# Optimization experiments

Hardware: AMD Instinct MI355X
Metric: run time of the kernel (lower is better)

The kernel has to match this reference:

```python
import jax, jax.numpy as jnp
import numpy as np

N, E, R = 30000, 480000, 8192
N_IN, E_IN = 128, 64
N_HID, E_HID = 256, 128
N_OUT, E_OUT = 256, 64
N_CLASS, N_COL = 10, 128
NEG = 0.01  # LeakyReLU slope


def leaky(x):
    return jnp.where(x > 0, x, NEG * x)


def pe_init(n_pos, d):
    # sinusoid position encoding table (position_encoding_init)
    pe = np.array([[p / np.power(10000, 2 * (j // 2) / d) for j in range(d)]
                   if p != 0 else np.zeros(d) for p in range(n_pos)])
    pe[1:, 0::2] = np.sin(pe[1:, 0::2])
    pe[1:, 1::2] = np.cos(pe[1:, 1::2])
    return jnp.asarray(pe, jnp.float32)


def segment_mean(vals, idx, n):
    s = jax.ops.segment_sum(vals, idx, num_segments=n)
    c = jax.ops.segment_sum(jnp.ones((vals.shape[0], 1), vals.dtype), idx, num_segments=n)
    return s / jnp.maximum(c, 1.0)


def esage(x, e, src, dst, We, be, Wn, bn):
    # edge update from [x_src ; e], mean-aggregate messages to dst nodes, node update
    e2 = leaky(jnp.concatenate([x[src], e], axis=-1) @ We + be)      # [E, e_out]
    h = segment_mean(e2, dst, x.shape[0])                             # [N, e_out]
    x2 = leaky(jnp.concatenate([x, h], axis=-1) @ Wn + bn)            # [N, n_out]
    return x2, e2


def setup_inputs():
    key = jax.random.key(0)
    ks = jax.random.split(key, 24)

    def xav(k, shp):
        std = float(np.sqrt(2.0 / (shp[0] + shp[1])))
        return jax.random.normal(k, shp, jnp.float32) * std

    return {
        'x': jax.random.normal(ks[0], (N, N_IN), jnp.float32),
        'e': jax.random.normal(ks[1], (E, E_IN), jnp.float32),
        'src': jax.random.randint(ks[2], (E,), 0, N),
        'dst': jax.random.randint(ks[3], (E,), 0, N),
        'row_idx': jax.random.randint(ks[4], (R,), 0, N),
        'col_idx': jax.random.randint(ks[5], (N_COL,), 0, N),
        'real': jax.random.normal(ks[6], (R * N_COL, E_OUT), jnp.float32),
        'mask': jax.random.randint(ks[7], (R, N_COL), 0, 2) == 1,
        'W1e': xav(ks[8], (N_IN + E_IN, E_HID)), 'b1e': jnp.zeros((E_HID,), jnp.float32),
        'W1n': xav(ks[9], (N_IN + E_HID, N_HID)), 'b1n': jnp.zeros((N_HID,), jnp.float32),
        'W2e': xav(ks[10], (N_HID + E_HID, E_OUT)), 'b2e': jnp.zeros((E_OUT,), jnp.float32),
        'W2n': xav(ks[11], (N_HID + E_OUT, N_OUT)), 'b2n': jnp.zeros((N_OUT,), jnp.float32),
        'node_pe': pe_init(N_COL, N_HID),
        'Wq': xav(ks[12], (N_HID, N_HID)),
        'Wk': xav(ks[13], (N_HID, N_HID)),
        'Wv': xav(ks[14], (N_HID, N_HID)),
        'Wref': xav(ks[15], (N_HID, N_HID)), 'bref': jnp.zeros((N_HID,), jnp.float32),
        'Wr': xav(ks[16], (N_OUT, E_OUT)),
        'Wc': xav(ks[17], (N_HID, E_OUT)), 'bep': jnp.zeros((E_OUT,), jnp.float32),
        'Wcls': xav(ks[18], (N_COL * E_OUT, N_CLASS)), 'bcls': jnp.zeros((N_CLASS,), jnp.float32),
    }


def reference(x, e, src, dst, row_idx, col_idx, real, mask,
              W1e, b1e, W1n, b1n, W2e, b2e, W2n, b2n,
              node_pe, Wq, Wk, Wv, Wref, bref, Wr, Wc, bep, Wcls, bcls):
    # two ESAGE message-passing layers
    x1, e1 = esage(x, e, src, dst, W1e, b1e, W1n, b1n)
    new_col = x1[col_idx]                                  # [C, n_hidden]
    x2, e2 = esage(x1, e1, src, dst, W2e, b2e, W2n, b2n)
    new_row = x2[row_idx]                                  # [R, n_out]

    # node self-attention (hand-rolled, incl. the duplicated dist@v from the source)
    c = new_col + node_pe
    q, k, v = c @ Wq, c @ Wk, c @ Wv
    dist = jax.nn.softmax((q @ k.T) * (1.0 / np.sqrt(N_HID)), axis=-1)
    c = 2.0 * (dist @ v)                                    # mm(dist,v) + mm(dist,v)
    new_col = jax.nn.sigmoid(c @ Wref + bref)

    # edge predictor over all (row, col) pairs: [R, C, e_out]
    pred = leaky((new_row @ Wr)[:, None, :] + (new_col @ Wc)[None, :, :] + bep)
    pred_flat = pred.reshape(R * N_COL, E_OUT)

    # masked imputation: real where mask True, predicted elsewhere
    imput_e = jnp.where(mask.reshape(-1)[:, None], real, pred_flat)
    imput_e = imput_e.reshape(R, N_COL, E_OUT)

    # mlp classifier: Flatten -> Linear -> LogSoftmax
    res = jax.nn.log_softmax(imput_e.reshape(R, -1) @ Wcls + bcls, axis=-1)
    return (res, pred_flat)
```

## Files before the change

kernel.cpp:

```cpp
#include <hip/hip_runtime.h>
#include <hip/hip_bf16.h>
#include <math.h>

#define NNODES 30000
#define NEDGES 480000
#define RROWS  8192
#define NCOLS  128
#define NIN    128
#define EIN    64
#define NHID   256
#define EHID   128
#define NOUTD  256
#define EOUTD  64
#define NCLS   10
#define NB_PFX 118

typedef __attribute__((ext_vector_type(8))) unsigned short ushort8;
typedef __attribute__((ext_vector_type(8))) short bhalf8;
typedef __attribute__((ext_vector_type(4))) float floatx4;

__device__ __forceinline__ float lrelu(float v){ return v > 0.f ? v : 0.01f * v; }
__device__ __forceinline__ float4 ld4(const float* p){ return *(const float4*)p; }
__device__ __forceinline__ float4 ntld4(const float* p){
    floatx4 v = __builtin_nontemporal_load((const floatx4*)p);
    return make_float4(v.x, v.y, v.z, v.w);
}
__device__ __forceinline__ void ntst4(float* p, float4 v){
    floatx4 n = {v.x, v.y, v.z, v.w};
    __builtin_nontemporal_store(n, (floatx4*)p);
}
__device__ __forceinline__ void ntst8u(unsigned short* p, ushort8 v){
    __builtin_nontemporal_store(v, (ushort8*)p);
}
__device__ __forceinline__ unsigned short f2b(float f){
    unsigned int u = __builtin_bit_cast(unsigned int, f);
    u += 0x7fffu + ((u >> 16) & 1u);
    return (unsigned short)(u >> 16);
}
__device__ __forceinline__ float b2f(unsigned short b){
    unsigned int u = ((unsigned int)b) << 16;
    return __builtin_bit_cast(float, u);
}

#define PREP_CVT_N   1875
#define PREP_W1T_B   (PREP_CVT_N)
#define PREP_W1B_B   (PREP_W1T_B + 64)
#define PREP_W2T_B   (PREP_W1B_B + 32)
#define PREP_W2B_B   (PREP_W2T_B + 64)
#define PREP_W1N_B   (PREP_W2B_B + 32)
#define PREP_W2N_B   (PREP_W1N_B + 256)
#define PREP_HIST_B  (PREP_W2N_B + 320)
#define PREP_DET_B   (PREP_HIST_B + 1875)
#define PREP_TOTAL   (PREP_DET_B + 1)

__device__ __forceinline__ void wT_region(const float* __restrict__ W, unsigned short* __restrict__ Wt,
                                          int KOFF, int KSUB, int N, int idx){
    if (idx >= N * KSUB) return;
    int n = idx / KSUB, k = idx % KSUB;
    Wt[idx] = f2b(W[(size_t)(KOFF + k) * N + n]);
}

__global__ __launch_bounds__(256) void k_prep(
    const float* __restrict__ x, unsigned short* __restrict__ xb,
    const float* __restrict__ W1e, unsigned short* __restrict__ W1tT, unsigned short* __restrict__ W1bT,
    const float* __restrict__ W2e, unsigned short* __restrict__ W2tT, unsigned short* __restrict__ W2bT,
    const float* __restrict__ W1n, unsigned short* __restrict__ W1nTb,
    const float* __restrict__ W2n, unsigned short* __restrict__ W2nTb,
    const int* __restrict__ dst, int* __restrict__ cnt_i,
    const unsigned int* __restrict__ mask, int* __restrict__ mode)
{
    const int bid = blockIdx.x, t = threadIdx.x;
    if (bid < PREP_CVT_N){
        int i = bid * 256 + t;
        float4 a = ntld4(x + (size_t)i * 8), b = ntld4(x + (size_t)i * 8 + 4);
        ushort8 o = {f2b(a.x), f2b(a.y), f2b(a.z), f2b(a.w), f2b(b.x), f2b(b.y), f2b(b.z), f2b(b.w)};
        *(ushort8*)(xb + (size_t)i * 8) = o;
    } else if (bid < PREP_W1B_B){
        wT_region(W1e, W1tT, 0, 128, 128, (bid - PREP_W1T_B) * 256 + t);
    } else if (bid < PREP_W2T_B){
        wT_region(W1e, W1bT, 128, 64, 128, (bid - PREP_W1B_B) * 256 + t);
    } else if (bid < PREP_W2B_B){
        wT_region(W2e, W2tT, 0, 256, 64, (bid - PREP_W2T_B) * 256 + t);
    } else if (bid < PREP_W1N_B){
        wT_region(W2e, W2bT, 256, 128, 64, (bid - PREP_W2B_B) * 256 + t);
    } else if (bid < PREP_W2N_B){
        wT_region(W1n, W1nTb, 0, 256, 256, (bid - PREP_W1N_B) * 256 + t);
    } else if (bid < PREP_HIST_B){
        wT_region(W2n, W2nTb, 0, 320, 256, (bid - PREP_W2N_B) * 256 + t);
    } else if (bid < PREP_DET_B){
        int i = (bid - PREP_HIST_B) * 256 + t;
        if (i < NEDGES) atomicAdd(&cnt_i[dst[i]], 1);
    } else if (t == 0){
        bool allI32 = true, allF32 = true;
        for (int i = 0; i < 64; i++){
            unsigned int v = mask[i];
            if (!(v == 0u || v == 1u)) allI32 = false;
            if (!(v == 0u || v == 0x3F800000u)) allF32 = false;
        }
        *mode = allI32 ? 0 : (allF32 ? 1 : 2);
    }
}

__global__ __launch_bounds__(256) void k_pfx1(const int* __restrict__ cnt_i, int* __restrict__ blocksum){
    __shared__ int red[256];
    const int t = threadIdx.x;
    const int i = blockIdx.x * 256 + t;
    red[t] = (i < NNODES) ? cnt_i[i] : 0;
    __syncthreads();
    for (int o = 128; o; o >>= 1){ if (t < o) red[t] += red[t + o]; __syncthreads(); }
    if (t == 0) blocksum[blockIdx.x] = red[0];
}
__global__ __launch_bounds__(128) void k_pfx2(const int* __restrict__ blocksum, int* __restrict__ blockoff){
    __shared__ int s[128];
    const int t = threadIdx.x;
    int v = (t < NB_PFX) ? blocksum[t] : 0;
    s[t] = v;
    __syncthreads();
    for (int o = 1; o < 128; o <<= 1){
        int add = (t >= o) ? s[t - o] : 0;
        __syncthreads();
        s[t] += add;
        __syncthreads();
    }
    if (t < NB_PFX) blockoff[t] = s[t] - v;
}
__global__ __launch_bounds__(256) void k_pfx3(const int* __restrict__ cnt_i, const int* __restrict__ blockoff,
                                              int* __restrict__ cursor, float* __restrict__ cntf){
    __shared__ int s[256];
    const int t = threadIdx.x;
    const int i = blockIdx.x * 256 + t;
    int v = (i < NNODES) ? cnt_i[i] : 0;
    s[t] = v;
    __syncthreads();
    for (int o = 1; o < 256; o <<= 1){
        int add = (t >= o) ? s[t - o] : 0;
        __syncthreads();
        s[t] += add;
        __syncthreads();
    }
    if (i < NNODES){
        cursor[i] = s[t] - v + blockoff[blockIdx.x];
        cntf[i] = (float)v;
    }
}

__global__ void k_scatter(const int* __restrict__ dst, int* __restrict__ cursor, int* __restrict__ eidx){
    int i = blockIdx.x * 256 + threadIdx.x;
    if (i >= NEDGES) return;
    int pos = atomicAdd(&cursor[dst[i]], 1);
    eidx[pos] = i;
}
__global__ void k_sgather(const int* __restrict__ src, const int* __restrict__ dst,
                          const int* __restrict__ eidx,
                          int* __restrict__ srcs, int* __restrict__ dsts){
    int p = blockIdx.x * 256 + threadIdx.x;
    if (p >= NEDGES) return;
    int i = eidx[p];
    srcs[p] = src[i];
    dsts[p] = dst[i];
}

template<int K, int N>
__global__ __launch_bounds__(256) void k_gemm_b16(
    const unsigned short* __restrict__ Ab, const unsigned short* __restrict__ Wt,
    unsigned short* __restrict__ outb, int M)
{
    __shared__ unsigned short At[64][K + 8];
    const int t = threadIdx.x;
    const int r0 = blockIdx.x * 64;
    {
        const int r = t >> 2, q = t & 3;
        const int row = r0 + r;
        const bool valid = row < M;
        const unsigned short* a = Ab + (size_t)(valid ? row : 0) * K;
        for (int kk = q * (K / 4); kk < (q + 1) * (K / 4); kk += 8){
            ushort8 u;
            if (valid) u = *(const ushort8*)(a + kk);
            else       u = (ushort8){0,0,0,0,0,0,0,0};
            *(ushort8*)&At[r][kk] = u;
        }
    }
    __syncthreads();
    const int lane = t & 63, w = t >> 6;
    const int fr = lane & 15, fq = lane >> 4;
    constexpr int NF = N / 16;
    floatx4 acc[NF] = {};
    #pragma unroll
    for (int ks = 0; ks < K / 32; ks++){
        const int k = ks * 32 + fq * 8;
        bhalf8 a = *(bhalf8*)&At[w * 16 + fr][k];
        #pragma unroll
        for (int n = 0; n < NF; n++){
            bhalf8 b = *(const bhalf8*)(Wt + (size_t)(n * 16 + fr) * K + k);
            acc[n] = __builtin_amdgcn_mfma_f32_16x16x32_bf16(a, b, acc[n], 0, 0, 0);
        }
    }
    #pragma unroll
    for (int n = 0; n < NF; n++){
        const int col = n * 16 + fr;
        #pragma unroll
        for (int rr = 0; rr < 4; rr++){
            const int row = r0 + w * 16 + fq * 4 + rr;
            if (row < M) outb[(size_t)row * N + col] = f2b(acc[n][rr]);
        }
    }
}

__global__ __launch_bounds__(256) void k_edge1_fused(
    const float* __restrict__ e,
    const int* __restrict__ srcs, const int* __restrict__ dsts, const int* __restrict__ eidx,
    const unsigned short* __restrict__ W1bT, const float* __restrict__ b1e,
    const unsigned short* __restrict__ P1b, const unsigned short* __restrict__ W2bT,
    unsigned short* __restrict__ Qb, float* __restrict__ hsum)
{
    __shared__ unsigned short Cb[64][136];
    __shared__ unsigned short P1s[64][136];
    __shared__ int dstS[64];
    const int t = threadIdx.x;
    const int p0 = blockIdx.x * 64;
    const int r = t >> 2, q = t & 3;
    {
        const int p = p0 + r;
        if (q == 0) dstS[r] = dsts[p];
        const int srow = srcs[p];
        const unsigned short* pp = P1b + (size_t)srow * 128 + q * 32;
        *(ushort8*)&P1s[r][q * 32]      = *(const ushort8*)pp;
        *(ushort8*)&P1s[r][q * 32 + 8]  = *(const ushort8*)(pp + 8);
        *(ushort8*)&P1s[r][q * 32 + 16] = *(const ushort8*)(pp + 16);
        *(ushort8*)&P1s[r][q * 32 + 24] = *(const ushort8*)(pp + 24);
        const int ei = eidx[p];
        const float* ep = e + (size_t)ei * 64 + q * 16;
        float4 f0 = ntld4(ep), f1 = ntld4(ep + 4), f2 = ntld4(ep + 8), f3 = ntld4(ep + 12);
        ushort8 u0 = {f2b(f0.x), f2b(f0.y), f2b(f0.z), f2b(f0.w), f2b(f1.x), f2b(f1.y), f2b(f1.z), f2b(f1.w)};
        ushort8 u1 = {f2b(f2.x), f2b(f2.y), f2b(f2.z), f2b(f2.w), f2b(f3.x), f2b(f3.y), f2b(f3.z), f2b(f3.w)};
        *(ushort8*)&Cb[r][q * 16]     = u0;
        *(ushort8*)&Cb[r][q * 16 + 8] = u1;
    }
    __syncthreads();
    const int lane = t & 63, w = t >> 6;
    const int wm = w >> 1, wn = w & 1;
    const int fr = lane & 15, fq = lane >> 4;
    floatx4 acc1[2][4] = {};
    #pragma unroll
    for (int ks = 0; ks < 2; ks++){
        const int k = ks * 32 + fq * 8;
        bhalf8 a0 = *(bhalf8*)&Cb[wm * 32 + fr][k];
        bhalf8 a1 = *(bhalf8*)&Cb[wm * 32 + 16 + fr][k];
        #pragma unroll
        for (int n = 0; n < 4; n++){
            const int col = wn * 64 + n * 16 + fr;
            bhalf8 b = *(const bhalf8*)(W1bT + (size_t)col * 64 + k);
            acc1[0][n] = __builtin_amdgcn_mfma_f32_16x16x32_bf16(a0, b, acc1[0][n], 0, 0, 0);
            acc1[1][n] = __builtin_amdgcn_mfma_f32_16x16x32_bf16(a1, b, acc1[1][n], 0, 0, 0);
        }
    }
    __syncthreads();
    #pragma unroll
    for (int m = 0; m < 2; m++){
        #pragma unroll
        for (int n = 0; n < 4; n++){
            const int col = wn * 64 + n * 16 + fr;
            const float bv = b1e[col];
            #pragma unroll
            for (int rr = 0; rr < 4; rr++){
                const int row = wm * 32 + m * 16 + fq * 4 + rr;
                const float pv = b2f(P1s[row][col]);
                Cb[row][col] = f2b(lrelu(acc1[m][n][rr] + pv + bv));
            }
        }
    }
    __syncthreads();
    {
        floatx4 acc2[4] = {};
        #pragma unroll
        for (int ks = 0; ks < 4; ks++){
            const int k = ks * 32 + fq * 8;
            bhalf8 a = *(bhalf8*)&Cb[w * 16 + fr][k];
            #pragma unroll
            for (int n = 0; n < 4; n++){
                bhalf8 b = *(const bhalf8*)(W2bT + (size_t)(n * 16 + fr) * 128 + k);
                acc2[n] = __builtin_amdgcn_mfma_f32_16x16x32_bf16(a, b, acc2[n], 0, 0, 0);
            }
        }
        #pragma unroll
        for (int n = 0; n < 4; n++){
            const int col = n * 16 + fr;
            #pragma unroll
            for (int rr = 0; rr < 4; rr++){
                const int row = w * 16 + fq * 4 + rr;
                P1s[row][col] = f2b(acc2[n][rr]);
            }
        }
    }
    __syncthreads();
    {
        unsigned short* op = Qb + (size_t)(p0 + r) * 64 + q * 16;
        ntst8u(op,     *(ushort8*)&P1s[r][q * 16]);
        ntst8u(op + 8, *(ushort8*)&P1s[r][q * 16 + 8]);
    }
    {
        const int col = t & 127, half = t >> 7;
        const int rbase = half * 32;
        float s = 0.f;
        int prev = dstS[rbase];
        #pragma unroll 4
        for (int rr = 0; rr < 32; rr++){
            const int rw2 = rbase + rr;
            const int d = dstS[rw2];
            if (d != prev){
                atomicAdd(&hsum[(size_t)prev * EHID + col], s);
                s = 0.f; prev = d;
            }
            s += b2f(Cb[rw2][col]);
        }
        atomicAdd(&hsum[(size_t)prev * EHID + col], s);
    }
}

__global__ __launch_bounds__(256) void k_edge2_lite(
    const unsigned short* __restrict__ P2b, const unsigned short* __restrict__ Qb,
    const int* __restrict__ srcs, const int* __restrict__ dsts,
    const float* __restrict__ b2e, float* __restrict__ hsum)
{
    const int t = threadIdx.x;
    const int lane = t & 63, w = t >> 6;
    const int p0 = blockIdx.x * 256 + w * 64;
    const float bias = b2e[lane];
    float s = 0.f;
    int prev = dsts[p0];
    #pragma unroll 4
    for (int i = 0; i < 64; i++){
        const int p = p0 + i;
        const int d = dsts[p];
        if (d != prev){
            atomicAdd(&hsum[(size_t)prev * EOUTD + lane], s);
            s = 0.f; prev = d;
        }
        const float q  = b2f(__builtin_nontemporal_load(&Qb[(size_t)p * 64 + lane]));
        const float pv = b2f(P2b[(size_t)srcs[p] * 64 + lane]);
        s += lrelu(pv + q + bias);
    }
    atomicAdd(&hsum[(size_t)prev * EOUTD + lane], s);
}

template<int K1, int K2, bool WRITE_BF16>
__global__ __launch_bounds__(256) void k_node_mfma(
    const unsigned short* __restrict__ A1b, const float* __restrict__ hsum,
    const float* __restrict__ cntf,
    const unsigned short* __restrict__ Wt, const float* __restrict__ bias,
    float* __restrict__ outf, unsigned short* __restrict__ outb, int M)
{
    constexpr int K = K1 + K2;
    __shared__ unsigned short At[32][K + 8];
    const int t = threadIdx.x;
    const int r0 = blockIdx.x * 32;
    {
        const int r = t >> 3, q = t & 7;
        const int row = r0 + r;
        const bool valid = row < M;
        float rinv = 0.f;
        const unsigned short* a1 = A1b;
        const float* a2 = hsum;
        if (valid){
            rinv = 1.f / fmaxf(cntf[row], 1.f);
            a1 = A1b  + (size_t)row * K1;
            a2 = hsum + (size_t)row * K2;
        }
        for (int kk = q * (K / 8); kk < (q + 1) * (K / 8); kk += 8){
            ushort8 u;
            if (!valid){
                u = (ushort8){0,0,0,0,0,0,0,0};
            } else if (kk < K1){
                u = *(const ushort8*)(a1 + kk);
            } else {
                float4 f0 = ld4(a2 + (kk - K1)), f1 = ld4(a2 + (kk - K1) + 4);
                u = (ushort8){f2b(f0.x*rinv), f2b(f0.y*rinv), f2b(f0.z*rinv), f2b(f0.w*rinv),
                              f2b(f1.x*rinv), f2b(f1.y*rinv), f2b(f1.z*rinv), f2b(f1.w*rinv)};
            }
            *(ushort8*)&At[r][kk] = u;
        }
    }
    __syncthreads();
    const int lane = t & 63, w = t >> 6;
    const int wm = w >> 1, wn = w & 1;
    const int fr = lane & 15, fq = lane >> 4;
    floatx4 acc[8] = {};
    #pragma unroll
    for (int ks = 0; ks < K / 32; ks++){
        const int k = ks * 32 + fq * 8;
        bhalf8 a = *(bhalf8*)&At[wm * 16 + fr][k];
        #pragma unroll
        for (int n = 0; n < 8; n++){
            const int col = wn * 128 + n * 16 + fr;
            bhalf8 b = *(const bhalf8*)(Wt + (size_t)col * K + k);
            acc[n] = __builtin_amdgcn_mfma_f32_16x16x32_bf16(a, b, acc[n], 0, 0, 0);
        }
    }
    #pragma unroll
    for (int n = 0; n < 8; n++){
        const int col = wn * 128 + n * 16 + fr;
        const float bv = bias[col];
        #pragma unroll
        for (int rr = 0; rr < 4; rr++){
            const int row = r0 + wm * 16 + fq * 4 + rr;
            if (row < M){
                float o = lrelu(acc[n][rr] + bv);
                outf[(size_t)row * 256 + col] = o;
                if (WRITE_BF16) outb[(size_t)row * 256 + col] = f2b(o);
            }
        }
    }
}

__global__ __launch_bounds__(256) void k_attn_qkv(
    const float* __restrict__ x1, const int* __restrict__ col_idx,
    const float* __restrict__ pe,
    const float* __restrict__ Wq, const float* __restrict__ Wk, const float* __restrict__ Wv,
    float* __restrict__ qo, float* __restrict__ ko, float* __restrict__ vo)
{
    __shared__ float c[256];
    const int i = blockIdx.x, t = threadIdx.x;
    const int col = col_idx[i];
    c[t] = x1[(size_t)col * 256 + t] + pe[i * 256 + t];
    __syncthreads();
    float aq = 0.f, ak = 0.f, av = 0.f;
    #pragma unroll 4
    for (int kk = 0; kk < 256; kk++){
        float cv = c[kk];
        aq += cv * Wq[kk * 256 + t];
        ak += cv * Wk[kk * 256 + t];
        av += cv * Wv[kk * 256 + t];
    }
    qo[i * 256 + t] = aq; ko[i * 256 + t] = ak; vo[i * 256 + t] = av;
}

__global__ __launch_bounds__(128) void k_attn_dist(
    const float* __restrict__ q, const float* __restrict__ k, float* __restrict__ dist)
{
    __shared__ float qr[256];
    __shared__ float red[128];
    const int i = blockIdx.x, t = threadIdx.x;
    qr[t] = q[i * 256 + t]; qr[t + 128] = q[i * 256 + t + 128];
    __syncthreads();
    float s = 0.f;
    #pragma unroll 4
    for (int kk = 0; kk < 256; kk++) s += qr[kk] * k[t * 256 + kk];
    s *= 0.0625f;
    red[t] = s; __syncthreads();
    for (int off = 64; off; off >>= 1){ if (t < off) red[t] = fmaxf(red[t], red[t + off]); __syncthreads(); }
    float m = red[0]; __syncthreads();
    float ex = expf(s - m);
    red[t] = ex; __syncthreads();
    for (int off = 64; off; off >>= 1){ if (t < off) red[t] += red[t + off]; __syncthreads(); }
    dist[i * 128 + t] = ex / red[0];
}

__global__ __launch_bounds__(256) void k_attn_out(
    const float* __restrict__ dist, const float* __restrict__ v,
    const float* __restrict__ Wref, const float* __restrict__ bref,
    const float* __restrict__ Wc, const float* __restrict__ bep,
    float* __restrict__ colWc)
{
    __shared__ float dr[128];
    __shared__ float c2[256];
    __shared__ float nc[256];
    const int i = blockIdx.x, t = threadIdx.x;
    if (t < 128) dr[t] = dist[i * 128 + t];
    __syncthreads();
    float s = 0.f;
    #pragma unroll 4
    for (int j = 0; j < 128; j++) s += dr[j] * v[j * 256 + t];
    c2[t] = 2.f * s;
    __syncthreads();
    float a = 0.f;
    #pragma unroll 4
    for (int kk = 0; kk < 256; kk++) a += c2[kk] * Wref[kk * 256 + t];
    a += bref[t];
    nc[t] = 1.f / (1.f + expf(-a));
    __syncthreads();
    if (t < 64){
        float o = 0.f;
        #pragma unroll 4
        for (int kk = 0; kk < 256; kk++) o += nc[kk] * Wc[kk * 64 + t];
        colWc[i * 64 + t] = o + bep[t];
    }
}

__global__ __launch_bounds__(256) void k_rowwr(
    const float* __restrict__ x2, const int* __restrict__ row_idx,
    const float* __restrict__ Wr, float* __restrict__ rw)
{
    __shared__ float A[16][260];
    const int t = threadIdx.x;
    const int r0 = blockIdx.x * 16;
    const int rl = t >> 4, cg = t & 15;
    const int ridx = row_idx[r0 + rl];
    const float* ar = x2 + (size_t)ridx * 256;
    for (int i = cg; i < 64; i += 16) *(float4*)(&A[rl][i * 4]) = ld4(ar + i * 4);
    __syncthreads();
    float acc[4] = {0.f, 0.f, 0.f, 0.f};
    #pragma unroll 4
    for (int kk = 0; kk < 256; kk++){
        float4 w = ld4(Wr + (size_t)kk * 64 + cg * 4);
        float a = A[rl][kk];
        acc[0] += a * w.x; acc[1] += a * w.y; acc[2] += a * w.z; acc[3] += a * w.w;
    }
    *(float4*)(rw + (size_t)(r0 + rl) * 64 + cg * 4) = make_float4(acc[0], acc[1], acc[2], acc[3]);
}

__global__ __launch_bounds__(256) void k_pred8(
    const float* __restrict__ rowWr, const float* __restrict__ colWc,
    const void* __restrict__ maskp, const int* __restrict__ modep,
    const float* __restrict__ real, const float* __restrict__ Wcls, const float* __restrict__ bcls,
    float* __restrict__ out)
{
    __shared__ float colWc_s[8192];
    __shared__ float rowWr_s[8 * 64];
    __shared__ unsigned char mask_s[8 * 128];
    __shared__ float part[4][80];
    __shared__ float logits_s[80];
    const int t  = threadIdx.x;
    const int r0 = blockIdx.x * 8;
    const int mode = *modep;
    for (int idx = t; idx < 2048; idx += 256)
        *(float4*)&colWc_s[idx * 4] = ld4(colWc + idx * 4);
    for (int idx = t; idx < 128; idx += 256)
        *(float4*)&rowWr_s[idx * 4] = ld4(rowWr + (size_t)r0 * 64 + idx * 4);
    for (int idx = t; idx < 1024; idx += 256){
        const int g = idx >> 7, c = idx & 127;
        const int gi = (r0 + g) * 128 + c;
        bool m;
        if (mode == 2)      m = ((const unsigned char*)maskp)[gi] != 0;
        else if (mode == 0) m = ((const int*)maskp)[gi] != 0;
        else                m = ((const float*)maskp)[gi] != 0.f;
        mask_s[idx] = m ? 1 : 0;
    }
    __syncthreads();

    float acc[8][10];
    #pragma unroll
    for (int g = 0; g < 8; g++)
        #pragma unroll
        for (int c = 0; c < 10; c++) acc[g][c] = 0.f;
    float* pred = out + RROWS * NCLS;

    #pragma unroll 1
    for (int i = 0; i < 8; i++){
        const int e4   = i * 256 + t;
        const int base = e4 * 4;
        const int c = base >> 6;
        const int j = base & 63;
        float4 cw = ld4(&colWc_s[c * 64 + j]);
        float w40[40];
        #pragma unroll
        for (int u = 0; u < 10; u++){
            float4 wv = ld4(Wcls + (size_t)base * 10 + u * 4);
            w40[u*4+0] = wv.x; w40[u*4+1] = wv.y; w40[u*4+2] = wv.z; w40[u*4+3] = wv.w;
        }
        #pragma unroll
        for (int g = 0; g < 8; g++){
            const int rr = r0 + g;
            float4 rwv = ld4(&rowWr_s[g * 64 + j]);
            float4 p;
            p.x = lrelu(rwv.x + cw.x); p.y = lrelu(rwv.y + cw.y);
            p.z = lrelu(rwv.z + cw.z); p.w = lrelu(rwv.w + cw.w);
            ntst4(pred + (size_t)rr * 8192 + base, p);
            float4 im = p;
            if (mask_s[g * 128 + c]) im = ntld4(real + (size_t)rr * 8192 + base);
            #pragma unroll
            for (int cls = 0; cls < 10; cls++){
                acc[g][cls] += im.x * w40[cls]      + im.y * w40[10 + cls]
                             + im.z * w40[20 + cls] + im.w * w40[30 + cls];
            }
        }
    }
    #pragma unroll
    for (int g = 0; g < 8; g++)
        #pragma unroll
        for (int cls = 0; cls < 10; cls++){
            float v = acc[g][cls];
            for (int off = 32; off; off >>= 1) v += __shfl_down(v, off, 64);
            acc[g][cls] = v;
        }
    const int wid = t >> 6, lane = t & 63;
    if (lane == 0){
        #pragma unroll
        for (int g = 0; g < 8; g++)
            #pragma unroll
            for (int cls = 0; cls < 10; cls++) part[wid][g * 10 + cls] = acc[g][cls];
    }
    __syncthreads();
    if (t < 80) logits_s[t] = part[0][t] + part[1][t] + part[2][t] + part[3][t] + bcls[t % 10];
    __syncthreads();
    if (t < 8){
        float m = -1e30f;
        #pragma unroll
        for (int cls = 0; cls < 10; cls++) m = fmaxf(m, logits_s[t * 10 + cls]);
        float se = 0.f;
        #pragma unroll
        for (int cls = 0; cls < 10; cls++) se += expf(logits_s[t * 10 + cls] - m);
        float ls = logf(se) + m;
        #pragma unroll
        for (int cls = 0; cls < 10; cls++) out[(r0 + t) * 10 + cls] = logits_s[t * 10 + cls] - ls;
    }
}

extern "C" void kernel_launch(void* const* d_in, const int* in_sizes, int n_in,
                              void* d_out, int out_size, void* d_ws, size_t ws_size,
                              hipStream_t stream)
{
    const float* x      = (const float*)d_in[0];
    const float* e      = (const float*)d_in[1];
    const int*   src    = (const int*)d_in[2];
    const int*   dst    = (const int*)d_in[3];
    const int*   row_idx= (const int*)d_in[4];
    const int*   col_idx= (const int*)d_in[5];
    const float* real   = (const float*)d_in[6];
    const void*  mask   = d_in[7];
    const float* W1e    = (const float*)d_in[8];
    const float* b1e    = (const float*)d_in[9];
    const float* W1n    = (const float*)d_in[10];
    const float* b1n    = (const float*)d_in[11];
    const float* W2e    = (const float*)d_in[12];
    const float* b2e    = (const float*)d_in[13];
    const float* W2n    = (const float*)d_in[14];
    const float* b2n    = (const float*)d_in[15];
    const float* pe     = (const float*)d_in[16];
    const float* Wq     = (const float*)d_in[17];
    const float* Wk     = (const float*)d_in[18];
    const float* Wv     = (const float*)d_in[19];
    const float* Wref   = (const float*)d_in[20];
    const float* bref   = (const float*)d_in[21];
    const float* Wr     = (const float*)d_in[22];
    const float* Wc     = (const float*)d_in[23];
    const float* bep    = (const float*)d_in[24];
    const float* Wcls   = (const float*)d_in[25];
    const float* bcls   = (const float*)d_in[26];

    float* ws = (float*)d_ws;
    size_t off = 0;
    float* h1sum = ws + off; off += (size_t)NNODES * EHID;
    float* h2sum = ws + off; off += (size_t)NNODES * EOUTD;
    int*   cnt_i = (int*)(ws + off); off += NNODES;
    const size_t zero_floats = off;
    float* cntf  = ws + off; off += NNODES;
    int*   cursor= (int*)(ws + off); off += NNODES;
    int*   srcs  = (int*)(ws + off); off += NEDGES;
    int*   dsts  = (int*)(ws + off); off += NEDGES;
    int*   eidx  = (int*)(ws + off); off += NEDGES;
    float* x1    = ws + off; off += (size_t)NNODES * NHID;
    float* x2    = ws + off; off += (size_t)NNODES * NOUTD;
    unsigned short* xb    = (unsigned short*)(ws + off); off += (size_t)NNODES * NIN  / 2;
    unsigned short* x1b   = (unsigned short*)(ws + off); off += (size_t)NNODES * NHID / 2;
    unsigned short* W1tT  = (unsigned short*)(ws + off); off += 128 * 128 / 2;
    unsigned short* W1bT  = (unsigned short*)(ws + off); off += 128 * 64 / 2;
    unsigned short* W2tT  = (unsigned short*)(ws + off); off += 64 * 256 / 2;
    unsigned short* W2bT  = (unsigned short*)(ws + off); off += 64 * 128 / 2;
    unsigned short* W1nTb = (unsigned short*)(ws + off); off += 256 * 256 / 2;
    unsigned short* W2nTb = (unsigned short*)(ws + off); off += 256 * 320 / 2;
    unsigned short* P1b   = (unsigned short*)(ws + off); off += (size_t)NNODES * 128 / 2;
    unsigned short* P2b   = (unsigned short*)(ws + off); off += (size_t)NNODES * 64 / 2;
    float* qb    = ws + off; off += 128 * 256;
    float* kb    = ws + off; off += 128 * 256;
    float* vb    = ws + off; off += 128 * 256;
    float* distb = ws + off; off += 128 * 128;
    float* colWc = ws + off; off += 128 * 64;
    float* rowWrb= ws + off; off += (size_t)RROWS * EOUTD;
    int*   modep = (int*)(ws + off); off += 4;
    int*   blocksum = (int*)(ws + off); off += 128;
    int*   blockoff = (int*)(ws + off); off += 128;
    unsigned short* Qb;
    size_t need = (off + (size_t)NEDGES * 32) * sizeof(float);
    if (ws_size >= need) Qb = (unsigned short*)(ws + off);
    else                 Qb = (unsigned short*)((float*)d_out + (size_t)RROWS * NCLS);

    (void)hipMemsetAsync(d_ws, 0, zero_floats * sizeof(float), stream);
    k_prep<<<PREP_TOTAL, 256, 0, stream>>>(x, xb, W1e, W1tT, W1bT, W2e, W2tT, W2bT,
                                           W1n, W1nTb, W2n, W2nTb, dst, cnt_i,
                                           (const unsigned int*)mask, modep);
    k_pfx1<<<NB_PFX, 256, 0, stream>>>(cnt_i, blocksum);
    k_pfx2<<<1, 128, 0, stream>>>(blocksum, blockoff);
    k_pfx3<<<NB_PFX, 256, 0, stream>>>(cnt_i, blockoff, cursor, cntf);
    k_scatter<<<(NEDGES + 255) / 256, 256, 0, stream>>>(dst, cursor, eidx);
    k_sgather<<<(NEDGES + 255) / 256, 256, 0, stream>>>(src, dst, eidx, srcs, dsts);
    k_gemm_b16<128, 128><<<(NNODES + 63) / 64, 256, 0, stream>>>(xb, W1tT, P1b, NNODES);
    k_edge1_fused<<<NEDGES / 64, 256, 0, stream>>>(e, srcs, dsts, eidx, W1bT, b1e, P1b, W2bT, Qb, h1sum);
    k_node_mfma<NIN, EHID, true><<<(NNODES + 31) / 32, 256, 0, stream>>>(xb, h1sum, cntf, W1nTb, b1n, x1, x1b, NNODES);
    k_gemm_b16<256, 64><<<(NNODES + 63) / 64, 256, 0, stream>>>(x1b, W2tT, P2b, NNODES);
    k_edge2_lite<<<NEDGES / 256, 256, 0, stream>>>(P2b, Qb, srcs, dsts, b2e, h2sum);
    k_node_mfma<NHID, EOUTD, false><<<(NNODES + 31) / 32, 256, 0, stream>>>(x1b, h2sum, cntf, W2nTb, b2n, x2, (unsigned short*)nullptr, NNODES);
    k_attn_qkv<<<128, 256, 0, stream>>>(x1, col_idx, pe, Wq, Wk, Wv, qb, kb, vb);
    k_attn_dist<<<128, 128, 0, stream>>>(qb, kb, distb);
    k_attn_out<<<128, 256, 0, stream>>>(distb, vb, Wref, bref, Wc, bep, colWc);
    k_rowwr<<<RROWS / 16, 256, 0, stream>>>(x2, row_idx, Wr, rowWrb);
    k_pred8<<<RROWS / 8, 256, 0, stream>>>(rowWrb, colWc, mask, modep, real, Wcls, bcls, (float*)d_out);
}
```

Measured before the change: 611.3 us.

## Fuse node1 with P2 projection, double-tile edge1 with prefetch, drop fp32 node outputs

Edge1 now handles two 64-edge tiles per block and register-prefetches the second tile's gathered inputs while the first tile's MFMAs run. The layer-1 node GEMM is fused with the P2 projection GEMM by reusing its bf16 output held in shared memory, which removes one launch and one read of x1b. The fp32 copies of x1 and x2 are dropped, so attention and row projection read bf16 activations, cutting memory traffic. The cost is slightly lower precision in the attention and row paths and more register pressure in the edge kernel.

```diff
diff --git a/kernel.cpp b/kernel.cpp
--- a/kernel.cpp
+++ b/kernel.cpp
@@ -217,103 +217,130 @@
     __shared__ unsigned short P1s[64][136];
     __shared__ int dstS[64];
     const int t = threadIdx.x;
-    const int p0 = blockIdx.x * 64;
     const int r = t >> 2, q = t & 3;
-    {
-        const int p = p0 + r;
-        if (q == 0) dstS[r] = dsts[p];
-        const int srow = srcs[p];
-        const unsigned short* pp = P1b + (size_t)srow * 128 + q * 32;
-        *(ushort8*)&P1s[r][q * 32]      = *(const ushort8*)pp;
-        *(ushort8*)&P1s[r][q * 32 + 8]  = *(const ushort8*)(pp + 8);
-        *(ushort8*)&P1s[r][q * 32 + 16] = *(const ushort8*)(pp + 16);
-        *(ushort8*)&P1s[r][q * 32 + 24] = *(const ushort8*)(pp + 24);
-        const int ei = eidx[p];
-        const float* ep = e + (size_t)ei * 64 + q * 16;
-        float4 f0 = ntld4(ep), f1 = ntld4(ep + 4), f2 = ntld4(ep + 8), f3 = ntld4(ep + 12);
-        ushort8 u0 = {f2b(f0.x), f2b(f0.y), f2b(f0.z), f2b(f0.w), f2b(f1.x), f2b(f1.y), f2b(f1.z), f2b(f1.w)};
-        ushort8 u1 = {f2b(f2.x), f2b(f2.y), f2b(f2.z), f2b(f2.w), f2b(f3.x), f2b(f3.y), f2b(f3.z), f2b(f3.w)};
-        *(ushort8*)&Cb[r][q * 16]     = u0;
-        *(ushort8*)&Cb[r][q * 16 + 8] = u1;
-    }
-    __syncthreads();
     const int lane = t & 63, w = t >> 6;
     const int wm = w >> 1, wn = w & 1;
     const int fr = lane & 15, fq = lane >> 4;
-    floatx4 acc1[2][4] = {};
+    const int base = blockIdx.x * 128;
+
+    float4 f0, f1, f2, f3;
+    ushort8 u0, u1, u2, u3;
+    int dcur;
+
+    {
+        const int p = base + r;
+        dcur = dsts[p];
+        const int srow = srcs[p];
+        const int ei = eidx[p];
+        const float* ep = e + (size_t)ei * 64 + q * 16;
+        f0 = ntld4(ep); f1 = ntld4(ep + 4); f2 = ntld4(ep + 8); f3 = ntld4(ep + 12);
+        const unsigned short* pp = P1b + (size_t)srow * 128 + q * 32;
+        u0 = *(const ushort8*)pp;       u1 = *(const ushort8*)(pp + 8);
+        u2 = *(const ushort8*)(pp + 16); u3 = *(const ushort8*)(pp + 24);
+    }
+
     #pragma unroll
-    for (int ks = 0; ks < 2; ks++){
-        const int k = ks * 32 + fq * 8;
-        bhalf8 a0 = *(bhalf8*)&Cb[wm * 32 + fr][k];
-        bhalf8 a1 = *(bhalf8*)&Cb[wm * 32 + 16 + fr][k];
-        #pragma unroll
-        for (int n = 0; n < 4; n++){
-            const int col = wn * 64 + n * 16 + fr;
-            bhalf8 b = *(const bhalf8*)(W1bT + (size_t)col * 64 + k);
-            acc1[0][n] = __builtin_amdgcn_mfma_f32_16x16x32_bf16(a0, b, acc1[0][n], 0, 0, 0);
-            acc1[1][n] = __builtin_amdgcn_mfma_f32_16x16x32_bf16(a1, b, acc1[1][n], 0, 0, 0);
-        }
-    }
-    __syncthreads();
-    #pragma unroll
-    for (int m = 0; m < 2; m++){
-        #pragma unroll
-        for (int n = 0; n < 4; n++){
-            const int col = wn * 64 + n * 16 + fr;
-            const float bv = b1e[col];
-            #pragma unroll
-            for (int rr = 0; rr < 4; rr++){
-                const int row = wm * 32 + m * 16 + fq * 4 + rr;
-                const float pv = b2f(P1s[row][col]);
-                Cb[row][col] = f2b(lrelu(acc1[m][n][rr] + pv + bv));
-            }
-        }
-    }
-    __syncthreads();
-    {
-        floatx4 acc2[4] = {};
-        #pragma unroll
-        for (int ks = 0; ks < 4; ks++){
+    for (int tile = 0; tile < 2; tile++){
+        const int p0 = base + tile * 64;
+        if (tile) __syncthreads();
+        if (q == 0) dstS[r] = dcur;
+        {
+            ushort8 e0 = {f2b(f0.x), f2b(f0.y), f2b(f0.z), f2b(f0.w), f2b(f1.x), f2b(f1.y), f2b(f1.z), f2b(f1.w)};
+            ushort8 e1v = {f2b(f2.x), f2b(f2.y), f2b(f2.z), f2b(f2.w), f2b(f3.x), f2b(f3.y), f2b(f3.z), f2b(f3.w)};
+            *(ushort8*)&Cb[r][q * 16]     = e0;
+            *(ushort8*)&Cb[r][q * 16 + 8] = e1v;
+            *(ushort8*)&P1s[r][q * 32]      = u0;
+            *(ushort8*)&P1s[r][q * 32 + 8]  = u1;
+            *(ushort8*)&P1s[r][q * 32 + 16] = u2;
+            *(ushort8*)&P1s[r][q * 32 + 24] = u3;
+        }
+        __syncthreads();
+        if (tile == 0){
+            const int p = base + 64 + r;
+            dcur = dsts[p];
+            const int srow = srcs[p];
+            const int ei = eidx[p];
+            const float* ep = e + (size_t)ei * 64 + q * 16;
+            f0 = ntld4(ep); f1 = ntld4(ep + 4); f2 = ntld4(ep + 8); f3 = ntld4(ep + 12);
+            const unsigned short* pp = P1b + (size_t)srow * 128 + q * 32;
+            u0 = *(const ushort8*)pp;       u1 = *(const ushort8*)(pp + 8);
+            u2 = *(const ushort8*)(pp + 16); u3 = *(const ushort8*)(pp + 24);
+        }
+        floatx4 acc1[2][4] = {};
+        #pragma unroll
+        for (int ks = 0; ks < 2; ks++){
             const int k = ks * 32 + fq * 8;
-            bhalf8 a = *(bhalf8*)&Cb[w * 16 + fr][k];
+            bhalf8 a0 = *(bhalf8*)&Cb[wm * 32 + fr][k];
+            bhalf8 a1 = *(bhalf8*)&Cb[wm * 32 + 16 + fr][k];
             #pragma unroll
             for (int n = 0; n < 4; n++){
-                bhalf8 b = *(const bhalf8*)(W2bT + (size_t)(n * 16 + fr) * 128 + k);
-                acc2[n] = __builtin_amdgcn_mfma_f32_16x16x32_bf16(a, b, acc2[n], 0, 0, 0);
-            }
-        }
-        #pragma unroll
-        for (int n = 0; n < 4; n++){
-            const int col = n * 16 + fr;
+                const int col = wn * 64 + n * 16 + fr;
+                bhalf8 b = *(const bhalf8*)(W1bT + (size_t)col * 64 + k);
+                acc1[0][n] = __builtin_amdgcn_mfma_f32_16x16x32_bf16(a0, b, acc1[0][n], 0, 0, 0);
+                acc1[1][n] = __builtin_amdgcn_mfma_f32_16x16x32_bf16(a1, b, acc1[1][n], 0, 0, 0);
+            }
+        }
+        __syncthreads();
+        #pragma unroll
+        for (int m = 0; m < 2; m++){
             #pragma unroll
-            for (int rr = 0; rr < 4; rr++){
-                const int row = w * 16 + fq * 4 + rr;
-                P1s[row][col] = f2b(acc2[n][rr]);
-            }
-        }
-    }
-    __syncthreads();
-    {
-        unsigned short* op = Qb + (size_t)(p0 + r) * 64 + q * 16;
-        ntst8u(op,     *(ushort8*)&P1s[r][q * 16]);
-        ntst8u(op + 8, *(ushort8*)&P1s[r][q * 16 + 8]);
-    }
-    {
-        const int col = t & 127, half = t >> 7;
-        const int rbase = half * 32;
-        float s = 0.f;
-        int prev = dstS[rbase];
-        #pragma unroll 4
-        for (int rr = 0; rr < 32; rr++){
-            const int rw2 = rbase + rr;
-            const int d = dstS[rw2];
-            if (d != prev){
-                atomicAdd(&hsum[(size_t)prev * EHID + col], s);
-                s = 0.f; prev = d;
-            }
-            s += b2f(Cb[rw2][col]);
-        }
-        atomicAdd(&hsum[(size_t)prev * EHID + col], s);
+            for (int n = 0; n < 4; n++){
+                const int col = wn * 64 + n * 16 + fr;
+                const float bv = b1e[col];
+                #pragma unroll
+                for (int rr = 0; rr < 4; rr++){
+                    const int row = wm * 32 + m * 16 + fq * 4 + rr;
+                    const float pv = b2f(P1s[row][col]);
+                    Cb[row][col] = f2b(lrelu(acc1[m][n][rr] + pv + bv));
+                }
+            }
+        }
+        __syncthreads();
+        {
+            floatx4 acc2[4] = {};
+            #pragma unroll
+            for (int ks = 0; ks < 4; ks++){
+                const int k = ks * 32 + fq * 8;
+                bhalf8 a = *(bhalf8*)&Cb[w * 16 + fr][k];
+                #pragma unroll
+                for (int n = 0; n < 4; n++){
+                    bhalf8 b = *(const bhalf8*)(W2bT + (size_t)(n * 16 + fr) * 128 + k);
+                    acc2[n] = __builtin_amdgcn_mfma_f32_16x16x32_bf16(a, b, acc2[n], 0, 0, 0);
+                }
+            }
+            #pragma unroll
+            for (int n = 0; n < 4; n++){
+                const int col = n * 16 + fr;
+                #pragma unroll
+                for (int rr = 0; rr < 4; rr++){
+                    const int row = w * 16 + fq * 4 + rr;
+                    P1s[row][col] = f2b(acc2[n][rr]);
+                }
+            }
+        }
+        __syncthreads();
+        {
+            unsigned short* op = Qb + (size_t)(p0 + r) * 64 + q * 16;
+            ntst8u(op,     *(ushort8*)&P1s[r][q * 16]);
+            ntst8u(op + 8, *(ushort8*)&P1s[r][q * 16 + 8]);
+        }
+        {
+            const int col = t & 127, half = t >> 7;
+            const int rbase = half * 32;
+            float s = 0.f;
+            int prev = dstS[rbase];
+            #pragma unroll 4
+            for (int rr = 0; rr < 32; rr++){
+                const int rw2 = rbase + rr;
+                const int d = dstS[rw2];
+                if (d != prev){
+                    atomicAdd(&hsum[(size_t)prev * EHID + col], s);
+                    s = 0.f; prev = d;
+                }
+                s += b2f(Cb[rw2][col]);
+            }
+            atomicAdd(&hsum[(size_t)prev * EHID + col], s);
+        }
     }
 }
 
@@ -343,14 +370,14 @@
     atomicAdd(&hsum[(size_t)prev * EOUTD + lane], s);
 }
 
-template<int K1, int K2, bool WRITE_BF16>
-__global__ __launch_bounds__(256) void k_node_mfma(
+__global__ __launch_bounds__(256) void k_node1_p2(
     const unsigned short* __restrict__ A1b, const float* __restrict__ hsum,
     const float* __restrict__ cntf,
     const unsigned short* __restrict__ Wt, const float* __restrict__ bias,
-    float* __restrict__ outf, unsigned short* __restrict__ outb, int M)
-{
-    constexpr int K = K1 + K2;
+    const unsigned short* __restrict__ W2tT,
+    unsigned short* __restrict__ x1b, unsigned short* __restrict__ P2b, int M)
+{
+    constexpr int K = 256;
     __shared__ unsigned short At[32][K + 8];
     const int t = threadIdx.x;
     const int r0 = blockIdx.x * 32;
@@ -363,19 +390,19 @@
         const float* a2 = hsum;
         if (valid){
             rinv = 1.f / fmaxf(cntf[row], 1.f);
-            a1 = A1b  + (size_t)row * K1;
-            a2 = hsum + (size_t)row * K2;
-        }
-        for (int kk = q * (K / 8); kk < (q + 1) * (K / 8); kk += 8){
+            a1 = A1b  + (size_t)row * NIN;
+            a2 = hsum + (size_t)row * EHID;
+        }
+        for (int kk = q * 32; kk < q * 32 + 32; kk += 8){
             ushort8 u;
             if (!valid){
                 u = (ushort8){0,0,0,0,0,0,0,0};
-            } else if (kk < K1){
+            } else if (kk < NIN){
                 u = *(const ushort8*)(a1 + kk);
             } else {
-                float4 f0 = ld4(a2 + (kk - K1)), f1 = ld4(a2 + (kk - K1) + 4);
-                u = (ushort8){f2b(f0.x*rinv), f2b(f0.y*rinv), f2b(f0.z*rinv), f2b(f0.w*rinv),
-                              f2b(f1.x*rinv), f2b(f1.y*rinv), f2b(f1.z*rinv), f2b(f1.w*rinv)};
+                float4 g0 = ld4(a2 + (kk - NIN)), g1 = ld4(a2 + (kk - NIN) + 4);
+                u = (ushort8){f2b(g0.x*rinv), f2b(g0.y*rinv), f2b(g0.z*rinv), f2b(g0.w*rinv),
+                              f2b(g1.x*rinv), f2b(g1.y*rinv), f2b(g1.z*rinv), f2b(g1.w*rinv)};
             }
             *(ushort8*)&At[r][kk] = u;
         }
@@ -386,7 +413,7 @@
     const int fr = lane & 15, fq = lane >> 4;
     floatx4 acc[8] = {};
     #pragma unroll
-    for (int ks = 0; ks < K / 32; ks++){
+    for (int ks = 0; ks < 8; ks++){
         const int k = ks * 32 + fq * 8;
         bhalf8 a = *(bhalf8*)&At[wm * 16 + fr][k];
         #pragma unroll
@@ -396,6 +423,7 @@
             acc[n] = __builtin_amdgcn_mfma_f32_16x16x32_bf16(a, b, acc[n], 0, 0, 0);
         }
     }
+    __syncthreads();
     #pragma unroll
     for (int n = 0; n < 8; n++){
         const int col = wn * 128 + n * 16 + fr;
@@ -403,17 +431,103 @@
         #pragma unroll
         for (int rr = 0; rr < 4; rr++){
             const int row = r0 + wm * 16 + fq * 4 + rr;
-            if (row < M){
-                float o = lrelu(acc[n][rr] + bv);
-                outf[(size_t)row * 256 + col] = o;
-                if (WRITE_BF16) outb[(size_t)row * 256 + col] = f2b(o);
-            }
+            unsigned short ob = f2b(lrelu(acc[n][rr] + bv));
+            At[wm * 16 + fq * 4 + rr][col] = ob;
+            if (row < M) x1b[(size_t)row * 256 + col] = ob;
+        }
+    }
+    __syncthreads();
+    {
+        floatx4 acc2[2] = {};
+        #pragma unroll
+        for (int ks = 0; ks < 8; ks++){
+            const int k = ks * 32 + fq * 8;
+            bhalf8 a = *(bhalf8*)&At[wm * 16 + fr][k];
+            #pragma unroll
+            for (int n = 0; n < 2; n++){
+                const int col = wn * 32 + n * 16 + fr;
+                bhalf8 b = *(const bhalf8*)(W2tT + (size_t)col * 256 + k);
+                acc2[n] = __builtin_amdgcn_mfma_f32_16x16x32_bf16(a, b, acc2[n], 0, 0, 0);
+            }
+        }
+        #pragma unroll
+        for (int n = 0; n < 2; n++){
+            const int col = wn * 32 + n * 16 + fr;
+            #pragma unroll
+            for (int rr = 0; rr < 4; rr++){
+                const int row = r0 + wm * 16 + fq * 4 + rr;
+                if (row < M) P2b[(size_t)row * 64 + col] = f2b(acc2[n][rr]);
+            }
+        }
+    }
+}
+
+__global__ __launch_bounds__(256) void k_node2(
+    const unsigned short* __restrict__ A1b, const float* __restrict__ hsum,
+    const float* __restrict__ cntf,
+    const unsigned short* __restrict__ Wt, const float* __restrict__ bias,
+    unsigned short* __restrict__ outb, int M)
+{
+    constexpr int K = 320;
+    __shared__ unsigned short At[32][K + 8];
+    const int t = threadIdx.x;
+    const int r0 = blockIdx.x * 32;
+    {
+        const int r = t >> 3, q = t & 7;
+        const int row = r0 + r;
+        const bool valid = row < M;
+        float rinv = 0.f;
+        const unsigned short* a1 = A1b;
+        const float* a2 = hsum;
+        if (valid){
+            rinv = 1.f / fmaxf(cntf[row], 1.f);
+            a1 = A1b  + (size_t)row * NHID;
+            a2 = hsum + (size_t)row * EOUTD;
+        }
+        for (int kk = q * 40; kk < q * 40 + 40; kk += 8){
+            ushort8 u;
+            if (!valid){
+                u = (ushort8){0,0,0,0,0,0,0,0};
+            } else if (kk < NHID){
+                u = *(const ushort8*)(a1 + kk);
+            } else {
+                float4 g0 = ld4(a2 + (kk - NHID)), g1 = ld4(a2 + (kk - NHID) + 4);
+                u = (ushort8){f2b(g0.x*rinv), f2b(g0.y*rinv), f2b(g0.z*rinv), f2b(g0.w*rinv),
+                              f2b(g1.x*rinv), f2b(g1.y*rinv), f2b(g1.z*rinv), f2b(g1.w*rinv)};
+            }
+            *(ushort8*)&At[r][kk] = u;
+        }
+    }
+    __syncthreads();
+    const int lane = t & 63, w = t >> 6;
+    const int wm = w >> 1, wn = w & 1;
+    const int fr = lane & 15, fq = lane >> 4;
+    floatx4 acc[8] = {};
+    #pragma unroll
+    for (int ks = 0; ks < 10; ks++){
+        const int k = ks * 32 + fq * 8;
+        bhalf8 a = *(bhalf8*)&At[wm * 16 + fr][k];
+        #pragma unroll
+        for (int n = 0; n < 8; n++){
+            const int col = wn * 128 + n * 16 + fr;
+            bhalf8 b = *(const bhalf8*)(Wt + (size_t)col * K + k);
+            acc[n] = __builtin_amdgcn_mfma_f32_16x16x32_bf16(a, b, acc[n], 0, 0, 0);
+        }
+    }
+    #pragma unroll
+    for (int n = 0; n < 8; n++){
+        const int col = wn * 128 + n * 16 + fr;
+        const float bv = bias[col];
+        #pragma unroll
+        for (int rr = 0; rr < 4; rr++){
+            const int row = r0 + wm * 16 + fq * 4 + rr;
+            if (row < M) outb[(size_t)row * 256 + col] = f2b(lrelu(acc[n][rr] + bv));
         }
     }
 }
 
 __global__ __launch_bounds__(256) void k_attn_qkv(
-    const float* __restrict__ x1, const int* __restrict__ col_idx,
+    const unsigned short* __restrict__ x1b, const int* __restrict__ col_idx,
     const float* __restrict__ pe,
     const float* __restrict__ Wq, const float* __restrict__ Wk, const float* __restrict__ Wv,
     float* __restrict__ qo, float* __restrict__ ko, float* __restrict__ vo)
@@ -421,7 +535,7 @@
     __shared__ float c[256];
     const int i = blockIdx.x, t = threadIdx.x;
     const int col = col_idx[i];
-    c[t] = x1[(size_t)col * 256 + t] + pe[i * 256 + t];
+    c[t] = b2f(x1b[(size_t)col * 256 + t]) + pe[i * 256 + t];
     __syncthreads();
     float aq = 0.f, ak = 0.f, av = 0.f;
     #pragma unroll 4
@@ -487,22 +601,22 @@
 }
 
 __global__ __launch_bounds__(256) void k_rowwr(
-    const float* __restrict__ x2, const int* __restrict__ row_idx,
+    const unsigned short* __restrict__ x2b, const int* __restrict__ row_idx,
     const float* __restrict__ Wr, float* __restrict__ rw)
 {
-    __shared__ float A[16][260];
+    __shared__ unsigned short A[16][264];
     const int t = threadIdx.x;
     const int r0 = blockIdx.x * 16;
     const int rl = t >> 4, cg = t & 15;
     const int ridx = row_idx[r0 + rl];
-    const float* ar = x2 + (size_t)ridx * 256;
-    for (int i = cg; i < 64; i += 16) *(float4*)(&A[rl][i * 4]) = ld4(ar + i * 4);
+    const unsigned short* ar = x2b + (size_t)ridx * 256;
+    for (int i = cg; i < 32; i += 16) *(ushort8*)&A[rl][i * 8] = *(const ushort8*)(ar + i * 8);
     __syncthreads();
     float acc[4] = {0.f, 0.f, 0.f, 0.f};
     #pragma unroll 4
     for (int kk = 0; kk < 256; kk++){
         float4 w = ld4(Wr + (size_t)kk * 64 + cg * 4);
-        float a = A[rl][kk];
+        float a = b2f(A[rl][kk]);
         acc[0] += a * w.x; acc[1] += a * w.y; acc[2] += a * w.z; acc[3] += a * w.w;
     }
     *(float4*)(rw + (size_t)(r0 + rl) * 64 + cg * 4) = make_float4(acc[0], acc[1], acc[2], acc[3]);
@@ -648,10 +762,9 @@
     int*   srcs  = (int*)(ws + off); off += NEDGES;
     int*   dsts  = (int*)(ws + off); off += NEDGES;
     int*   eidx  = (int*)(ws + off); off += NEDGES;
-    float* x1    = ws + off; off += (size_t)NNODES * NHID;
-    float* x2    = ws + off; off += (size_t)NNODES * NOUTD;
     unsigned short* xb    = (unsigned short*)(ws + off); off += (size_t)NNODES * NIN  / 2;
     unsigned short* x1b   = (unsigned short*)(ws + off); off += (size_t)NNODES * NHID / 2;
+    unsigned short* x2b   = (unsigned short*)(ws + off); off += (size_t)NNODES * NOUTD / 2;
     unsigned short* W1tT  = (unsigned short*)(ws + off); off += 128 * 128 / 2;
     unsigned short* W1bT  = (unsigned short*)(ws + off); off += 128 * 64 / 2;
     unsigned short* W2tT  = (unsigned short*)(ws + off); off += 64 * 256 / 2;
@@ -684,14 +797,13 @@
     k_scatter<<<(NEDGES + 255) / 256, 256, 0, stream>>>(dst, cursor, eidx);
     k_sgather<<<(NEDGES + 255) / 256, 256, 0, stream>>>(src, dst, eidx, srcs, dsts);
     k_gemm_b16<128, 128><<<(NNODES + 63) / 64, 256, 0, stream>>>(xb, W1tT, P1b, NNODES);
-    k_edge1_fused<<<NEDGES / 64, 256, 0, stream>>>(e, srcs, dsts, eidx, W1bT, b1e, P1b, W2bT, Qb, h1sum);
-    k_node_mfma<NIN, EHID, true><<<(NNODES + 31) / 32, 256, 0, stream>>>(xb, h1sum, cntf, W1nTb, b1n, x1, x1b, NNODES);
-    k_gemm_b16<256, 64><<<(NNODES + 63) / 64, 256, 0, stream>>>(x1b, W2tT, P2b, NNODES);
+    k_edge1_fused<<<NEDGES / 128, 256, 0, stream>>>(e, srcs, dsts, eidx, W1bT, b1e, P1b, W2bT, Qb, h1sum);
+    k_node1_p2<<<(NNODES + 31) / 32, 256, 0, stream>>>(xb, h1sum, cntf, W1nTb, b1n, W2tT, x1b, P2b, NNODES);
     k_edge2_lite<<<NEDGES / 256, 256, 0, stream>>>(P2b, Qb, srcs, dsts, b2e, h2sum);
-    k_node_mfma<NHID, EOUTD, false><<<(NNODES + 31) / 32, 256, 0, stream>>>(x1b, h2sum, cntf, W2nTb, b2n, x2, (unsigned short*)nullptr, NNODES);
-    k_attn_qkv<<<128, 256, 0, stream>>>(x1, col_idx, pe, Wq, Wk, Wv, qb, kb, vb);
+    k_node2<<<(NNODES + 31) / 32, 256, 0, stream>>>(x1b, h2sum, cntf, W2nTb, b2n, x2b, NNODES);
+    k_attn_qkv<<<128, 256, 0, stream>>>(x1b, col_idx, pe, Wq, Wk, Wv, qb, kb, vb);
     k_attn_dist<<<128, 128, 0, stream>>>(qb, kb, distb);
     k_attn_out<<<128, 256, 0, stream>>>(distb, vb, Wref, bref, Wc, bep, colWc);
-    k_rowwr<<<RROWS / 16, 256, 0, stream>>>(x2, row_idx, Wr, rowWrb);
+    k_rowwr<<<RROWS / 16, 256, 0, stream>>>(x2b, row_idx, Wr, rowWrb);
     k_pred8<<<RROWS / 8, 256, 0, stream>>>(rowWrb, colWc, mask, modep, real, Wcls, bcls, (float*)d_out);
 }
```

After: 627.1 us. 2.6% more time.
